# Kernel optimization log

Hardware: AMD Instinct MI355X
Metric: run time of the kernel (lower is better)

## Reference

```python
import jax, jax.numpy as jnp
import numpy as np

D_MODEL = 1024
NHEAD = 16
HEAD_DIM = D_MODEL // NHEAD
WINDOW = 33  # mask keeps |i-j| > WINDOW//2 (True = attend, matching torch SDPA bool-mask semantics)


def setup_inputs() -> dict:
    key = jax.random.key(0)
    ks = jax.random.split(key, 9)
    s = 1.0 / np.sqrt(D_MODEL)
    x = jax.random.normal(ks[0], (2, 2048, D_MODEL), dtype=jnp.float32)
    Wq = jax.random.uniform(ks[1], (D_MODEL, D_MODEL), jnp.float32, -s, s)
    bq = jax.random.uniform(ks[2], (D_MODEL,), jnp.float32, -s, s)
    Wk = jax.random.uniform(ks[3], (D_MODEL, D_MODEL), jnp.float32, -s, s)
    bk = jax.random.uniform(ks[4], (D_MODEL,), jnp.float32, -s, s)
    Wv = jax.random.uniform(ks[5], (D_MODEL, D_MODEL), jnp.float32, -s, s)
    bv = jax.random.uniform(ks[6], (D_MODEL,), jnp.float32, -s, s)
    Wo = jax.random.uniform(ks[7], (D_MODEL, D_MODEL), jnp.float32, -s, s)
    bo = jax.random.uniform(ks[8], (D_MODEL,), jnp.float32, -s, s)
    return {"x": x, "Wq": Wq, "bq": bq, "Wk": Wk, "bk": bk,
            "Wv": Wv, "bv": bv, "Wo": Wo, "bo": bo}


def reference(x, Wq, bq, Wk, bk, Wv, bv, Wo, bo):
    B, T, C = x.shape
    H, D = NHEAD, HEAD_DIM
    # projections (torch Linear: y = x @ W.T + b)
    q = (x @ Wq.T + bq).reshape(B, T, H, D).transpose(0, 2, 1, 3)  # [B,H,T,D]
    k = (x @ Wk.T + bk).reshape(B, T, H, D).transpose(0, 2, 1, 3)
    v = (x @ Wv.T + bv).reshape(B, T, H, D).transpose(0, 2, 1, 3)
    idx = jnp.arange(T)
    rel = jnp.abs(idx[:, None] - idx[None, :])
    keep = rel > (WINDOW // 2)  # True = participate (torch SDPA bool-mask semantics)
    scale = 1.0 / jnp.sqrt(jnp.asarray(D, dtype=x.dtype))
    scores = jnp.einsum('bhqd,bhkd->bhqk', q, k) * scale
    scores = jnp.where(keep, scores, jnp.asarray(-jnp.inf, dtype=scores.dtype))
    attn = jax.nn.softmax(scores, axis=-1)
    out = jnp.einsum('bhqk,bhkd->bhqd', attn, v)  # [B,H,T,D]
    out = out.transpose(0, 2, 1, 3).reshape(B, T, C)
    return out @ Wo.T + bo
```

## Files before the change

kernel.cpp:

```cpp
#include <hip/hip_runtime.h>
#include <stdint.h>


typedef unsigned short u16;
typedef short bf16x8 __attribute__((ext_vector_type(8)));
typedef float f32x4 __attribute__((ext_vector_type(4)));

#define MFMA16 __builtin_amdgcn_mfma_f32_16x16x32_bf16

__device__ __forceinline__ u16 f2bf(float f) {
  union { float f; uint32_t u; } v; v.f = f;
  return (u16)((v.u + 0x7fffu + ((v.u >> 16) & 1u)) >> 16);
}

__device__ __forceinline__ uint32_t cvt_pk_bf16(float lo, float hi) {
  uint32_t d;
  asm("v_cvt_pk_bf16_f32 %0, %1, %2" : "=v"(d) : "v"(lo), "v"(hi));
  return d;
}

__global__ void f2b_kernel(const float* __restrict__ in, u16* __restrict__ out, int n4) {
  int i = blockIdx.x * blockDim.x + threadIdx.x;
  if (i < n4) {
    float4 v = reinterpret_cast<const float4*>(in)[i];
    ushort4 o;
    o.x = f2bf(v.x); o.y = f2bf(v.y); o.z = f2bf(v.z); o.w = f2bf(v.w);
    reinterpret_cast<ushort4*>(out)[i] = o;
  }
}

__global__ void f2b4_kernel(const float* __restrict__ a, const float* __restrict__ b,
                            const float* __restrict__ c, const float* __restrict__ d,
                            u16* __restrict__ oa, u16* __restrict__ ob,
                            u16* __restrict__ oc, u16* __restrict__ od, int n4) {
  int i = blockIdx.x * blockDim.x + threadIdx.x;
  if (i >= n4) return;
  int w = blockIdx.y;
  const float* src = (w == 0) ? a : (w == 1) ? b : (w == 2) ? c : d;
  u16* dst = (w == 0) ? oa : (w == 1) ? ob : (w == 2) ? oc : od;
  float4 v = reinterpret_cast<const float4*>(src)[i];
  ushort4 o;
  o.x = f2bf(v.x); o.y = f2bf(v.y); o.z = f2bf(v.z); o.w = f2bf(v.w);
  reinterpret_cast<ushort4*>(dst)[i] = o;
}

#define GEMM_LOAD(REGA, REGB, A_, B_, KOFF)                                                        \
  do {                                                                                             \
    REGA##0 = *reinterpret_cast<const uint4*>(A_ + (size_t)(gm_base +  0) * 1024 + (KOFF) + sslot * 8); \
    REGA##1 = *reinterpret_cast<const uint4*>(A_ + (size_t)(gm_base + 32) * 1024 + (KOFF) + sslot * 8); \
    REGA##2 = *reinterpret_cast<const uint4*>(A_ + (size_t)(gm_base + 64) * 1024 + (KOFF) + sslot * 8); \
    REGA##3 = *reinterpret_cast<const uint4*>(A_ + (size_t)(gm_base + 96) * 1024 + (KOFF) + sslot * 8); \
    REGB##0 = *reinterpret_cast<const uint4*>(B_ + (size_t)(gn_base +  0) * 1024 + (KOFF) + sslot * 8); \
    REGB##1 = *reinterpret_cast<const uint4*>(B_ + (size_t)(gn_base + 32) * 1024 + (KOFF) + sslot * 8); \
    REGB##2 = *reinterpret_cast<const uint4*>(B_ + (size_t)(gn_base + 64) * 1024 + (KOFF) + sslot * 8); \
    REGB##3 = *reinterpret_cast<const uint4*>(B_ + (size_t)(gn_base + 96) * 1024 + (KOFF) + sslot * 8); \
  } while (0)

#define GEMM_PUBLISH()                                                                             \
  do {                                                                                             \
    *reinterpret_cast<uint4*>((char*)As + (srow +  0) * 144 + sslot * 16) = ar0;                   \
    *reinterpret_cast<uint4*>((char*)As + (srow + 32) * 144 + sslot * 16) = ar1;                   \
    *reinterpret_cast<uint4*>((char*)As + (srow + 64) * 144 + sslot * 16) = ar2;                   \
    *reinterpret_cast<uint4*>((char*)As + (srow + 96) * 144 + sslot * 16) = ar3;                   \
    *reinterpret_cast<uint4*>((char*)Bs + (srow +  0) * 144 + sslot * 16) = br0;                   \
    *reinterpret_cast<uint4*>((char*)Bs + (srow + 32) * 144 + sslot * 16) = br1;                   \
    *reinterpret_cast<uint4*>((char*)Bs + (srow + 64) * 144 + sslot * 16) = br2;                   \
    *reinterpret_cast<uint4*>((char*)Bs + (srow + 96) * 144 + sslot * 16) = br3;                   \
  } while (0)

#define GEMM_CORE(A_, B_, bm0_, bn0_)                                                              \
  constexpr int KP = 72;                                                                           \
  __shared__ __align__(16) u16 As[128 * KP];                                                       \
  __shared__ __align__(16) u16 Bs[128 * KP];                                                       \
  const int t = threadIdx.x;                                                                       \
  const int lane = t & 63;                                                                         \
  const int wv = t >> 6;                                                                           \
  const int wm = (wv >> 1) * 64;                                                                   \
  const int wn = (wv & 1) * 64;                                                                    \
  const int lg = lane >> 4;                                                                        \
  const int lr = lane & 15;                                                                        \
  const int srow = t >> 3;                               \
  const int sslot = t & 7;                                            \
  const int gm_base = bm0_ + srow;                                                                 \
  const int gn_base = bn0_ + srow;                                                                 \
  uint4 ar0, ar1, ar2, ar3, br0, br1, br2, br3;                                                    \
  f32x4 acc[4][4];                                                                                 \
  for (int i = 0; i < 4; ++i)                                                                      \
    for (int j = 0; j < 4; ++j) acc[i][j] = (f32x4)0.0f;                                           \
  GEMM_LOAD(ar, br, A_, B_, 0);                                                                    \
  for (int k0 = 0; k0 < 1024; k0 += 64) {                                                          \
    GEMM_PUBLISH();                                                                                \
    __syncthreads();                                                                               \
    if (k0 + 64 < 1024) GEMM_LOAD(ar, br, A_, B_, k0 + 64);                                        \
    for (int kk = 0; kk < 2; ++kk) {                                                               \
      bf16x8 af[4], bfr[4];                                                                        \
      for (int i = 0; i < 4; ++i)                                                                  \
        af[i] = *reinterpret_cast<const bf16x8*>(&As[(wm + i * 16 + lr) * KP + kk * 32 + lg * 8]); \
      for (int j = 0; j < 4; ++j)                                                                  \
        bfr[j] = *reinterpret_cast<const bf16x8*>(&Bs[(wn + j * 16 + lr) * KP + kk * 32 + lg * 8]);\
      for (int i = 0; i < 4; ++i)                                                                  \
        for (int j = 0; j < 4; ++j)                                                                \
          acc[i][j] = MFMA16(af[i], bfr[j], acc[i][j], 0, 0, 0);                                   \
    }                                                                                              \
    __syncthreads();                                                                               \
  }

__global__ __launch_bounds__(256) void gemm_qkv(
    const u16* __restrict__ A,
    const u16* __restrict__ Wqb, const u16* __restrict__ Wkb, const u16* __restrict__ Wvb,
    const float* __restrict__ bqp, const float* __restrict__ bkp, const float* __restrict__ bvp,
    u16* __restrict__ qo, u16* __restrict__ ko, u16* __restrict__ vo)
{
  const int bid = blockIdx.x + gridDim.x * blockIdx.y;
  const int sid = (bid & 7) * 96 + (bid >> 3);
  const int bm0 = (sid / 24) * 128;
  const int jy = sid % 24;
  const int sel = jy >> 3;
  const int bn0 = (jy & 7) * 128;

  const u16* Bw = (sel == 0) ? Wqb : (sel == 1) ? Wkb : Wvb;
  const float* bias = (sel == 0) ? bqp : (sel == 1) ? bkp : bvp;
  const float scale = (sel == 0) ? 0.125f : 1.0f;

  GEMM_CORE(A, Bw, bm0, bn0)

  for (int j = 0; j < 4; ++j) {
    int gn = bn0 + wn + j * 16 + lr;
    float bv = bias[gn];
    for (int i = 0; i < 4; ++i) {
      for (int r = 0; r < 4; ++r) {
        int gm = bm0 + wm + i * 16 + lg * 4 + r;
        float val = (acc[i][j][r] + bv) * scale;
        int b = gm >> 11, tt = gm & 2047;
        int h = gn >> 6,  d = gn & 63;
        u16 o = f2bf(val);
        if (sel == 0)
          qo[((size_t)(b * 16 + h) * 2048 + tt) * 64 + d] = o;
        else if (sel == 1)
          ko[((size_t)(b * 16 + h) * 2048 + tt) * 64 + d] = o;
        else
          vo[((size_t)(b * 16 + h) * 64 + d) * 2048 + tt] = o;
      }
    }
  }
}

__global__ __launch_bounds__(256) void gemm_out(
    const u16* __restrict__ A, const u16* __restrict__ Bw,
    const float* __restrict__ bias, float* __restrict__ outp)
{
  const int bm0 = blockIdx.x * 128;
  const int bn0 = blockIdx.y * 128;

  GEMM_CORE(A, Bw, bm0, bn0)

  for (int j = 0; j < 4; ++j) {
    int gn = bn0 + wn + j * 16 + lr;
    float bv = bias[gn];
    for (int i = 0; i < 4; ++i)
      for (int r = 0; r < 4; ++r) {
        int gm = bm0 + wm + i * 16 + lg * 4 + r;
        outp[(size_t)gm * 1024 + gn] = acc[i][j][r] + bv;
      }
  }
}

__global__ __launch_bounds__(256, 2) void attn_kernel(
    const u16* __restrict__ qb, const u16* __restrict__ kb,
    const u16* __restrict__ vtb, u16* __restrict__ ab)
{
  constexpr int KP = 72;
  __shared__ __align__(16) u16 Kb[2][64 * KP];
  __shared__ __align__(16) u16 Vb[2][64 * KP];
  __shared__ __align__(16) u16 Pl[4][32 * 64];

  const int bid = blockIdx.x + gridDim.x * blockIdx.y;
  const int sid = (bid & 7) * 64 + (bid >> 3);
  const int bx = sid & 15;
  const int bh = sid >> 4;

  const int t = threadIdx.x;
  const int lane = t & 63;
  const int wv = t >> 6;
  const int lg = lane >> 4, lr = lane & 15;
  const int q0 = bx * 128 + wv * 32;

  const u16* Qp = qb + (size_t)bh * 2048 * 64;
  const u16* Kp = kb + (size_t)bh * 2048 * 64;
  const u16* Vt = vtb + (size_t)bh * 64 * 2048;
  char* Pw = (char*)&Pl[wv][0];
  const int swz = (lr & 7) << 4;

  const int sl = lane & 7;
  const int r0 = wv * 16 + (lane >> 3);
  const int sdst0 = r0 * (KP * 2) + sl * 16;

  uint4 krA, krB, vrA, vrB;

#define ISSUE_LOADS(J0N)                                                                 \
  do {                                                                                   \
    krA = *reinterpret_cast<const uint4*>(Kp + (size_t)((J0N) + r0) * 64 + sl * 8);      \
    krB = *reinterpret_cast<const uint4*>(Kp + (size_t)((J0N) + r0 + 8) * 64 + sl * 8);  \
    vrA = *reinterpret_cast<const uint4*>(Vt + (size_t)r0 * 2048 + (J0N) + sl * 8);      \
    vrB = *reinterpret_cast<const uint4*>(Vt + (size_t)(r0 + 8) * 2048 + (J0N) + sl * 8);\
  } while (0)

#define WRITE_LDS(BUF)                                                                   \
  do {                                                                                   \
    *reinterpret_cast<uint4*>((char*)&Kb[BUF][0] + sdst0)                = krA;          \
    *reinterpret_cast<uint4*>((char*)&Kb[BUF][0] + sdst0 + 8 * KP * 2)   = krB;          \
    *reinterpret_cast<uint4*>((char*)&Vb[BUF][0] + sdst0)                = vrA;          \
    *reinterpret_cast<uint4*>((char*)&Vb[BUF][0] + sdst0 + 8 * KP * 2)   = vrB;          \
  } while (0)

  bf16x8 qf[2][2];
  for (int qi = 0; qi < 2; ++qi)
    for (int h = 0; h < 2; ++h)
      qf[qi][h] = *reinterpret_cast<const bf16x8*>(&Qp[(size_t)(q0 + qi * 16 + lr) * 64 + h * 32 + lg * 8]);

  f32x4 o[2][4];
  for (int qi = 0; qi < 2; ++qi)
    for (int d = 0; d < 4; ++d) o[qi][d] = (f32x4)0.0f;
  float m[2] = {-1e30f, -1e30f};
  float l[2] = {0.0f, 0.0f};

  ISSUE_LOADS(0);
  WRITE_LDS(0);
  __syncthreads();
  int cur = 0;

  for (int tt = 0; tt < 32; ++tt) {
    if (tt < 31) ISSUE_LOADS((tt + 1) * 64);
    const int j0 = tt * 64;

    f32x4 s[2][4];
    for (int kc = 0; kc < 4; ++kc) {
      bf16x8 kf0 = *reinterpret_cast<const bf16x8*>(&Kb[cur][(kc * 16 + lr) * KP + lg * 8]);
      bf16x8 kf1 = *reinterpret_cast<const bf16x8*>(&Kb[cur][(kc * 16 + lr) * KP + 32 + lg * 8]);
      for (int qi = 0; qi < 2; ++qi) {
        f32x4 z = (f32x4)0.0f;
        z = MFMA16(kf0, qf[qi][0], z, 0, 0, 0);
        z = MFMA16(kf1, qf[qi][1], z, 0, 0, 0);
        s[qi][kc] = z;
      }
    }
    if (j0 + 63 >= q0 - 16 && j0 <= q0 + 47) {
      for (int qi = 0; qi < 2; ++qi)
        for (int kc = 0; kc < 4; ++kc)
          for (int r = 0; r < 4; ++r) {
            int i = q0 + qi * 16 + lr;
            int j = j0 + kc * 16 + lg * 4 + r;
            int dd = i - j; if (dd < 0) dd = -dd;
            if (dd <= 16) s[qi][kc][r] = -1e38f;
          }
    }
    float pm[2];
    for (int qi = 0; qi < 2; ++qi) {
      f32x4 t4 = s[qi][0];
      t4 = __builtin_elementwise_max(t4, s[qi][1]);
      t4 = __builtin_elementwise_max(t4, s[qi][2]);
      t4 = __builtin_elementwise_max(t4, s[qi][3]);
      float x = fmaxf(fmaxf(t4[0], t4[1]), fmaxf(t4[2], t4[3]));
      x = fmaxf(x, __shfl_xor(x, 16));
      x = fmaxf(x, __shfl_xor(x, 32));
      pm[qi] = x;
    }
    bool need = (pm[0] > m[0] + 8.0f) || (pm[1] > m[1] + 8.0f);
    if (__any((int)need)) {
      for (int qi = 0; qi < 2; ++qi) {
        float mn = fmaxf(m[qi], pm[qi]);
        float a = __expf(m[qi] - mn);
        m[qi] = mn;
        l[qi] *= a;
        for (int d = 0; d < 4; ++d) o[qi][d] *= a;
      }
    }
    for (int qi = 0; qi < 2; ++qi) {
      float sum = 0.0f;
      int rowbase = (qi * 16 + lr) * 128;
      for (int kc = 0; kc < 4; ++kc) {
        float p0 = __expf(s[qi][kc][0] - m[qi]);
        float p1 = __expf(s[qi][kc][1] - m[qi]);
        float p2 = __expf(s[qi][kc][2] - m[qi]);
        float p3 = __expf(s[qi][kc][3] - m[qi]);
        sum += (p0 + p1) + (p2 + p3);
        uint2 pk;
        pk.x = cvt_pk_bf16(p0, p1);
        pk.y = cvt_pk_bf16(p2, p3);
        *reinterpret_cast<uint2*>(Pw + ((rowbase + kc * 32 + lg * 8) ^ swz)) = pk;
      }
      sum += __shfl_xor(sum, 16);
      sum += __shfl_xor(sum, 32);
      l[qi] += sum;
    }
    asm volatile("s_waitcnt lgkmcnt(0)" ::: "memory");
    for (int kh = 0; kh < 2; ++kh) {
      bf16x8 pa[2];
      for (int qi = 0; qi < 2; ++qi)
        pa[qi] = *reinterpret_cast<const bf16x8*>(
            Pw + (((qi * 16 + lr) * 128 + kh * 64 + lg * 16) ^ swz));
      for (int d = 0; d < 4; ++d) {
        bf16x8 vf = *reinterpret_cast<const bf16x8*>(
            &Vb[cur][(d * 16 + lr) * KP + kh * 32 + lg * 8]);
        for (int qi = 0; qi < 2; ++qi)
          o[qi][d] = MFMA16(vf, pa[qi], o[qi][d], 0, 0, 0);
      }
    }
    if (tt < 31) WRITE_LDS(cur ^ 1);
    __syncthreads();
    cur ^= 1;
  }

  int b = bh >> 4, h = bh & 15;
  for (int qi = 0; qi < 2; ++qi) {
    float inv = 1.0f / l[qi];
    size_t rowoff = ((size_t)b * 2048 + q0 + qi * 16 + lr) * 1024 + h * 64;
    for (int d = 0; d < 4; ++d) {
      uint2 pk;
      pk.x = cvt_pk_bf16(o[qi][d][0] * inv, o[qi][d][1] * inv);
      pk.y = cvt_pk_bf16(o[qi][d][2] * inv, o[qi][d][3] * inv);
      *reinterpret_cast<uint2*>(&ab[rowoff + d * 16 + lg * 4]) = pk;
    }
  }
#undef ISSUE_LOADS
#undef WRITE_LDS
}

extern "C" void kernel_launch(void* const* d_in, const int* in_sizes, int n_in,
                              void* d_out, int out_size, void* d_ws, size_t ws_size,
                              hipStream_t stream) {
  const float* x  = (const float*)d_in[0];
  const float* Wq = (const float*)d_in[1];
  const float* bq = (const float*)d_in[2];
  const float* Wk = (const float*)d_in[3];
  const float* bk = (const float*)d_in[4];
  const float* Wv = (const float*)d_in[5];
  const float* bv = (const float*)d_in[6];
  const float* Wo = (const float*)d_in[7];
  const float* bo = (const float*)d_in[8];

  u16* ws  = (u16*)d_ws;
  u16* xb  = ws;
  u16* wqb = ws + 4194304;
  u16* wkb = ws + 5242880;
  u16* wvb = ws + 6291456;
  u16* wob = ws + 7340032;
  u16* qbf = ws + 8388608;
  u16* kbf = ws + 12582912;
  u16* vbf = ws + 16777216;
  u16* ab  = xb;

  f2b_kernel<<<4096, 256, 0, stream>>>(x, xb, 1048576);
  f2b4_kernel<<<dim3(1024, 4), 256, 0, stream>>>(Wq, Wk, Wv, Wo, wqb, wkb, wvb, wob, 262144);

  gemm_qkv<<<dim3(32, 24), 256, 0, stream>>>(xb, wqb, wkb, wvb, bq, bk, bv, qbf, kbf, vbf);

  attn_kernel<<<dim3(16, 32), 256, 0, stream>>>(qbf, kbf, vbf, ab);

  gemm_out<<<dim3(32, 8), 256, 0, stream>>>(ab, wob, bo, (float*)d_out);
}
```

Baseline: 142.5 us.

## Halve attention query tile per wave, double grid, use exp2 softmax

The attention kernel now gives each wave 16 query rows instead of 32, doubling the grid to 1024 blocks and raising launch bounds to 3 blocks per CU. The P staging buffer shrinks to match, which lowers register and LDS use. The Q projection folds log2(e) into its scale so the softmax can use exp2f, and the rescale threshold is adjusted to match. The cost is that each K/V tile loaded into LDS is now reused by half as many query rows, so total K/V traffic and per-tile sync overhead double.

```diff
diff --git a/kernel.cpp b/kernel.cpp
--- a/kernel.cpp
+++ b/kernel.cpp
@@ -79,8 +79,8 @@
   const int wn = (wv & 1) * 64;                                                                    \
   const int lg = lane >> 4;                                                                        \
   const int lr = lane & 15;                                                                        \
-  const int srow = t >> 3;                               \
-  const int sslot = t & 7;                                            \
+  const int srow = t >> 3;                                                                         \
+  const int sslot = t & 7;                                                                         \
   const int gm_base = bm0_ + srow;                                                                 \
   const int gn_base = bn0_ + srow;                                                                 \
   uint4 ar0, ar1, ar2, ar3, br0, br1, br2, br3;                                                    \
@@ -120,7 +120,7 @@
 
   const u16* Bw = (sel == 0) ? Wqb : (sel == 1) ? Wkb : Wvb;
   const float* bias = (sel == 0) ? bqp : (sel == 1) ? bkp : bvp;
-  const float scale = (sel == 0) ? 0.125f : 1.0f;
+  const float scale = (sel == 0) ? 0.125f * 1.44269504f : 1.0f;
 
   GEMM_CORE(A, Bw, bm0, bn0)
 
@@ -165,25 +165,25 @@
   }
 }
 
-__global__ __launch_bounds__(256, 2) void attn_kernel(
+__global__ __launch_bounds__(256, 3) void attn_kernel(
     const u16* __restrict__ qb, const u16* __restrict__ kb,
     const u16* __restrict__ vtb, u16* __restrict__ ab)
 {
   constexpr int KP = 72;
   __shared__ __align__(16) u16 Kb[2][64 * KP];
   __shared__ __align__(16) u16 Vb[2][64 * KP];
-  __shared__ __align__(16) u16 Pl[4][32 * 64];
+  __shared__ __align__(16) u16 Pl[4][16 * 64];
 
   const int bid = blockIdx.x + gridDim.x * blockIdx.y;
-  const int sid = (bid & 7) * 64 + (bid >> 3);
-  const int bx = sid & 15;
-  const int bh = sid >> 4;
+  const int sid = (bid & 7) * 128 + (bid >> 3);
+  const int bx = sid & 31;
+  const int bh = sid >> 5;
 
   const int t = threadIdx.x;
   const int lane = t & 63;
   const int wv = t >> 6;
   const int lg = lane >> 4, lr = lane & 15;
-  const int q0 = bx * 128 + wv * 32;
+  const int q0 = bx * 64 + wv * 16;
 
   const u16* Qp = qb + (size_t)bh * 2048 * 64;
   const u16* Kp = kb + (size_t)bh * 2048 * 64;
@@ -213,16 +213,13 @@
     *reinterpret_cast<uint4*>((char*)&Vb[BUF][0] + sdst0 + 8 * KP * 2)   = vrB;          \
   } while (0)
 
-  bf16x8 qf[2][2];
-  for (int qi = 0; qi < 2; ++qi)
-    for (int h = 0; h < 2; ++h)
-      qf[qi][h] = *reinterpret_cast<const bf16x8*>(&Qp[(size_t)(q0 + qi * 16 + lr) * 64 + h * 32 + lg * 8]);
-
-  f32x4 o[2][4];
-  for (int qi = 0; qi < 2; ++qi)
-    for (int d = 0; d < 4; ++d) o[qi][d] = (f32x4)0.0f;
-  float m[2] = {-1e30f, -1e30f};
-  float l[2] = {0.0f, 0.0f};
+  bf16x8 qf0 = *reinterpret_cast<const bf16x8*>(&Qp[(size_t)(q0 + lr) * 64 + lg * 8]);
+  bf16x8 qf1 = *reinterpret_cast<const bf16x8*>(&Qp[(size_t)(q0 + lr) * 64 + 32 + lg * 8]);
+
+  f32x4 o[4];
+  for (int d = 0; d < 4; ++d) o[d] = (f32x4)0.0f;
+  float m = -1e30f;
+  float lsum = 0.0f;
 
   ISSUE_LOADS(0);
   WRITE_LDS(0);
@@ -233,77 +230,55 @@
     if (tt < 31) ISSUE_LOADS((tt + 1) * 64);
     const int j0 = tt * 64;
 
-    f32x4 s[2][4];
+    f32x4 s[4];
     for (int kc = 0; kc < 4; ++kc) {
       bf16x8 kf0 = *reinterpret_cast<const bf16x8*>(&Kb[cur][(kc * 16 + lr) * KP + lg * 8]);
       bf16x8 kf1 = *reinterpret_cast<const bf16x8*>(&Kb[cur][(kc * 16 + lr) * KP + 32 + lg * 8]);
-      for (int qi = 0; qi < 2; ++qi) {
-        f32x4 z = (f32x4)0.0f;
-        z = MFMA16(kf0, qf[qi][0], z, 0, 0, 0);
-        z = MFMA16(kf1, qf[qi][1], z, 0, 0, 0);
-        s[qi][kc] = z;
-      }
-    }
-    if (j0 + 63 >= q0 - 16 && j0 <= q0 + 47) {
-      for (int qi = 0; qi < 2; ++qi)
-        for (int kc = 0; kc < 4; ++kc)
-          for (int r = 0; r < 4; ++r) {
-            int i = q0 + qi * 16 + lr;
-            int j = j0 + kc * 16 + lg * 4 + r;
-            int dd = i - j; if (dd < 0) dd = -dd;
-            if (dd <= 16) s[qi][kc][r] = -1e38f;
-          }
-    }
-    float pm[2];
-    for (int qi = 0; qi < 2; ++qi) {
-      f32x4 t4 = s[qi][0];
-      t4 = __builtin_elementwise_max(t4, s[qi][1]);
-      t4 = __builtin_elementwise_max(t4, s[qi][2]);
-      t4 = __builtin_elementwise_max(t4, s[qi][3]);
-      float x = fmaxf(fmaxf(t4[0], t4[1]), fmaxf(t4[2], t4[3]));
-      x = fmaxf(x, __shfl_xor(x, 16));
-      x = fmaxf(x, __shfl_xor(x, 32));
-      pm[qi] = x;
-    }
-    bool need = (pm[0] > m[0] + 8.0f) || (pm[1] > m[1] + 8.0f);
-    if (__any((int)need)) {
-      for (int qi = 0; qi < 2; ++qi) {
-        float mn = fmaxf(m[qi], pm[qi]);
-        float a = __expf(m[qi] - mn);
-        m[qi] = mn;
-        l[qi] *= a;
-        for (int d = 0; d < 4; ++d) o[qi][d] *= a;
-      }
-    }
-    for (int qi = 0; qi < 2; ++qi) {
-      float sum = 0.0f;
-      int rowbase = (qi * 16 + lr) * 128;
-      for (int kc = 0; kc < 4; ++kc) {
-        float p0 = __expf(s[qi][kc][0] - m[qi]);
-        float p1 = __expf(s[qi][kc][1] - m[qi]);
-        float p2 = __expf(s[qi][kc][2] - m[qi]);
-        float p3 = __expf(s[qi][kc][3] - m[qi]);
-        sum += (p0 + p1) + (p2 + p3);
-        uint2 pk;
-        pk.x = cvt_pk_bf16(p0, p1);
-        pk.y = cvt_pk_bf16(p2, p3);
-        *reinterpret_cast<uint2*>(Pw + ((rowbase + kc * 32 + lg * 8) ^ swz)) = pk;
-      }
-      sum += __shfl_xor(sum, 16);
-      sum += __shfl_xor(sum, 32);
-      l[qi] += sum;
+      f32x4 z = (f32x4)0.0f;
+      z = MFMA16(kf0, qf0, z, 0, 0, 0);
+      z = MFMA16(kf1, qf1, z, 0, 0, 0);
+      s[kc] = z;
+    }
+    if (j0 + 63 >= q0 - 16 && j0 <= q0 + 31) {
+      for (int kc = 0; kc < 4; ++kc)
+        for (int r = 0; r < 4; ++r) {
+          int i = q0 + lr;
+          int j = j0 + kc * 16 + lg * 4 + r;
+          int dd = i - j; if (dd < 0) dd = -dd;
+          if (dd <= 16) s[kc][r] = -1e38f;
+        }
+    }
+    f32x4 t4 = __builtin_elementwise_max(__builtin_elementwise_max(s[0], s[1]),
+                                         __builtin_elementwise_max(s[2], s[3]));
+    float pm = fmaxf(fmaxf(t4[0], t4[1]), fmaxf(t4[2], t4[3]));
+    pm = fmaxf(pm, __shfl_xor(pm, 16));
+    pm = fmaxf(pm, __shfl_xor(pm, 32));
+    if (__any((int)(pm > m + 11.54f))) {
+      float mn = fmaxf(m, pm);
+      float a = exp2f(m - mn);
+      m = mn;
+      lsum *= a;
+      for (int d = 0; d < 4; ++d) o[d] *= a;
+    }
+    for (int kc = 0; kc < 4; ++kc) {
+      float p0 = exp2f(s[kc][0] - m);
+      float p1 = exp2f(s[kc][1] - m);
+      float p2 = exp2f(s[kc][2] - m);
+      float p3 = exp2f(s[kc][3] - m);
+      lsum += (p0 + p1) + (p2 + p3);
+      uint2 pk;
+      pk.x = cvt_pk_bf16(p0, p1);
+      pk.y = cvt_pk_bf16(p2, p3);
+      *reinterpret_cast<uint2*>(Pw + ((lr * 128 + kc * 32 + lg * 8) ^ swz)) = pk;
     }
     asm volatile("s_waitcnt lgkmcnt(0)" ::: "memory");
     for (int kh = 0; kh < 2; ++kh) {
-      bf16x8 pa[2];
-      for (int qi = 0; qi < 2; ++qi)
-        pa[qi] = *reinterpret_cast<const bf16x8*>(
-            Pw + (((qi * 16 + lr) * 128 + kh * 64 + lg * 16) ^ swz));
+      bf16x8 pa = *reinterpret_cast<const bf16x8*>(
+          Pw + ((lr * 128 + kh * 64 + lg * 16) ^ swz));
       for (int d = 0; d < 4; ++d) {
         bf16x8 vf = *reinterpret_cast<const bf16x8*>(
             &Vb[cur][(d * 16 + lr) * KP + kh * 32 + lg * 8]);
-        for (int qi = 0; qi < 2; ++qi)
-          o[qi][d] = MFMA16(vf, pa[qi], o[qi][d], 0, 0, 0);
+        o[d] = MFMA16(vf, pa, o[d], 0, 0, 0);
       }
     }
     if (tt < 31) WRITE_LDS(cur ^ 1);
@@ -311,16 +286,16 @@
     cur ^= 1;
   }
 
+  lsum += __shfl_xor(lsum, 16);
+  lsum += __shfl_xor(lsum, 32);
+  float inv = 1.0f / lsum;
   int b = bh >> 4, h = bh & 15;
-  for (int qi = 0; qi < 2; ++qi) {
-    float inv = 1.0f / l[qi];
-    size_t rowoff = ((size_t)b * 2048 + q0 + qi * 16 + lr) * 1024 + h * 64;
-    for (int d = 0; d < 4; ++d) {
-      uint2 pk;
-      pk.x = cvt_pk_bf16(o[qi][d][0] * inv, o[qi][d][1] * inv);
-      pk.y = cvt_pk_bf16(o[qi][d][2] * inv, o[qi][d][3] * inv);
-      *reinterpret_cast<uint2*>(&ab[rowoff + d * 16 + lg * 4]) = pk;
-    }
+  size_t rowoff = ((size_t)b * 2048 + q0 + lr) * 1024 + h * 64;
+  for (int d = 0; d < 4; ++d) {
+    uint2 pk;
+    pk.x = cvt_pk_bf16(o[d][0] * inv, o[d][1] * inv);
+    pk.y = cvt_pk_bf16(o[d][2] * inv, o[d][3] * inv);
+    *reinterpret_cast<uint2*>(&ab[rowoff + d * 16 + lg * 4]) = pk;
   }
 #undef ISSUE_LOADS
 #undef WRITE_LDS
@@ -355,7 +330,7 @@
 
   gemm_qkv<<<dim3(32, 24), 256, 0, stream>>>(xb, wqb, wkb, wvb, bq, bk, bv, qbf, kbf, vbf);
 
-  attn_kernel<<<dim3(16, 32), 256, 0, stream>>>(qbf, kbf, vbf, ab);
+  attn_kernel<<<dim3(32, 32), 256, 0, stream>>>(qbf, kbf, vbf, ab);
 
   gemm_out<<<dim3(32, 8), 256, 0, stream>>>(ab, wob, bo, (float*)d_out);
 }
```

New measurement: 161.3 us. 1.13x slower.
